# Kernel optimization log

Measured on AMD Instinct MI355X. Metric: run time of the kernel, lower is better.

Reference implementation:

```python
import math
import jax, jax.numpy as jnp
import numpy as np

PERCENTAGES = [0.004, 0.006, 0.008, 0.01, 0.012]
RADIUS = 1.0          # init kwarg / uniform-loss radius
REPULSION_H = 0.0005  # h in get_repulsion_loss


def pairwise_sqdist(x, y):
    # x: [B,N,3], y: [B,M,3] -> [B,N,M] squared euclidean distances
    d2 = (jnp.sum(x * x, -1)[:, :, None]
          + jnp.sum(y * y, -1)[:, None, :]
          - 2.0 * jnp.einsum('bnd,bmd->bnm', x, y))
    return jnp.maximum(d2, 0.0)


def knn_sqdist(x, k):
    # sorted (ascending) squared distances to k nearest neighbors (incl. self)
    d2 = pairwise_sqdist(x, x)
    neg, _ = jax.lax.top_k(-d2, k)
    return -neg  # [B,N,k]


def fps(pcd, npoint):
    # furthest point sampling, start at index 0 (pn2 convention)
    B, N, _ = pcd.shape
    def step(carry, _):
        dist, last = carry
        p = jnp.take_along_axis(pcd, last[:, None, None], axis=1)  # [B,1,3]
        d = jnp.sum((pcd - p) ** 2, -1)                            # [B,N]
        dist = jnp.minimum(dist, d)
        nxt = jnp.argmax(dist, axis=-1)
        return (dist, nxt), nxt
    idx0 = jnp.zeros((B,), jnp.int32)
    dist0 = jnp.full((B, N), 1e10, pcd.dtype)
    _, rest = jax.lax.scan(step, (dist0, idx0), None, length=npoint - 1)
    return jnp.concatenate([idx0[None], rest], axis=0).T  # [B,npoint]


def ball_query(r, nsample, pcd, centers):
    # pn2 ball_query: first nsample indices with d2 < r^2, padded with first hit
    N = pcd.shape[1]
    d2 = pairwise_sqdist(centers, pcd)                       # [B,S,N]
    cand = jnp.where(d2 < r * r, jnp.arange(N)[None, None, :], N)
    sorted_idx = jnp.sort(cand, axis=-1)[..., :nsample]      # [B,S,nsample]
    first = sorted_idx[..., :1]
    return jnp.where(sorted_idx == N, first, sorted_idx)


def get_cd_loss(pred, gt, pcd_radius):
    d2 = pairwise_sqdist(gt, pred)       # [B,N,M]
    cost_for = jnp.min(d2, axis=2)       # gt -> pred, [B,N]
    cost_bac = jnp.min(d2, axis=1)       # pred -> gt, [B,M]
    cost = 0.8 * cost_for + 0.2 * cost_bac
    cost = cost / pcd_radius
    return jnp.mean(cost)


def get_repulsion_loss(pcd, h=REPULSION_H):
    d2 = knn_sqdist(pcd, 5)[:, :, 1:5]   # squared dists to 4 nearest (excl self)
    return jnp.mean(jnp.maximum(-d2 + h, 0.0))


def get_uniform_loss(pcd, radius=RADIUS):
    B, N, _ = pcd.shape
    npoint = int(N * 0.05)
    fidx = fps(pcd, npoint)
    new_xyz = jnp.take_along_axis(pcd, fidx[:, :, None], axis=1)  # [B,npoint,3]
    loss = 0.0
    for p in PERCENTAGES:
        nsample = int(N * p)
        r = math.sqrt(p * radius)
        disk_area = math.pi * radius ** 2 / N
        expect_len = math.sqrt(disk_area)
        idx = ball_query(r, nsample, pcd, new_xyz)            # [B,npoint,nsample]
        grouped = jax.vmap(lambda pts, i: pts[i])(pcd, idx)   # [B,npoint,nsample,3]
        grouped = grouped.reshape(B, npoint * nsample, 3)     # cat(unbind(dim=1))
        nn_d2 = knn_sqdist(grouped, 2)[:, :, 1:]              # [B,M,1]
        uniform_dist = jnp.abs(jnp.sqrt(nn_d2) + 1e-8)
        uniform_dist = jnp.mean(uniform_dist, axis=1)         # [B,1]
        uniform_dist = (uniform_dist - expect_len) ** 2 / (expect_len + 1e-8)
        loss = loss + jnp.mean(uniform_dist) * (p * 100.0) ** 2
    return loss / len(PERCENTAGES)


def setup_inputs() -> dict:
    key = jax.random.key(0)
    k1, k2 = jax.random.split(key)
    pred = jax.random.normal(k1, (8, 2048, 3), jnp.float32)
    gt = jax.random.normal(k2, (8, 2048, 3), jnp.float32)
    pcd_radius = jnp.ones((1,), jnp.float32)
    return {"pred": pred, "gt": gt, "pcd_radius": pcd_radius}


def reference(pred, gt, pcd_radius):
    cd = get_cd_loss(pred, gt, pcd_radius)
    rep = get_repulsion_loss(pred)
    uni = get_uniform_loss(pred)
    return cd + rep + uni
```

## Files before the change

kernel.cpp:

```cpp
#include <hip/hip_runtime.h>
#include <math.h>

#define BB 8
#define NN 2048
#define NPOINT 102
#define H_REP 0.0005f

typedef float v2f __attribute__((ext_vector_type(2)));

__device__ const int    c_ns[5] = {8, 12, 16, 20, 24};
__device__ const double c_p[5]  = {0.004, 0.006, 0.008, 0.01, 0.012};

#define OFF_CD 0
#define OFF_REP 512
#define OFF_UK 768
#define N_DBL 896

__device__ inline double aload_d(const double* p) {
    return __hip_atomic_load(p, __ATOMIC_RELAXED, __HIP_MEMORY_SCOPE_AGENT);
}

__device__ inline void ins5(float c, float& t0, float& t1, float& t2, float& t3, float& t4) {
    float lo;
    lo = fminf(t0, c); c = fmaxf(t0, c); t0 = lo;
    lo = fminf(t1, c); c = fmaxf(t1, c); t1 = lo;
    lo = fminf(t2, c); c = fmaxf(t2, c); t2 = lo;
    lo = fminf(t3, c); c = fmaxf(t3, c); t3 = lo;
    t4 = fminf(t4, c);
}

union SMemP1 {
    struct { float4 sB[NN]; float pm[2][4][128]; } cd;
    struct { float4 sP[NN]; float pm[2][4][64][5]; } rep;
    struct {
        float sx[2][NN], sy[2][NN], sz[2][NN];
        float2 sl[2][2][4];
        int sFi[2][NPOINT];
    } fps;
};

__global__ __launch_bounds__(512, 4) void k_phase1(const float* __restrict__ pred,
                                                   const float* __restrict__ gt,
                                                   int* __restrict__ fidx,
                                                   double* __restrict__ part,
                                                   int* __restrict__ done) {
    __shared__ SMemP1 sm;
    int bid = blockIdx.x;
    int tid = threadIdx.x;
    int lane = tid & 63, wid = tid >> 6;

    if (bid == 4 && tid == 0) *done = 0;

    if (bid < 4) {
        __builtin_amdgcn_s_setprio(1);
        int h = wid >> 2;
        int s = wid & 3;
        int b = bid * 2 + h;
        const float* pp = pred + (size_t)b * NN * 3;
        float px[8], py[8], pz[8], dist[8];
#pragma unroll
        for (int k = 0; k < 8; k++) {
            int i = (s << 9) + (k << 6) + lane;
            float x = pp[i * 3 + 0], y = pp[i * 3 + 1], z = pp[i * 3 + 2];
            px[k] = x; py[k] = y; pz[k] = z; dist[k] = 1e10f;
            sm.fps.sx[h][i] = x; sm.fps.sy[h][i] = y; sm.fps.sz[h][i] = z;
        }
        if ((tid & 255) == 0) sm.fps.sFi[h][0] = 0;
        __syncthreads();
        int last = 0;
#pragma unroll 1
        for (int step = 1; step < NPOINT; ++step) {
            float lx = sm.fps.sx[h][last], ly = sm.fps.sy[h][last], lz = sm.fps.sz[h][last];
            float bv = -1.0f;
            int bi = 0;
#pragma unroll
            for (int k = 0; k < 8; k++) {
                float dx = px[k] - lx, dy = py[k] - ly, dz = pz[k] - lz;
                float nd = fminf(dist[k], dx * dx + dy * dy + dz * dz);
                dist[k] = nd;
                bool better = nd > bv;
                bv = better ? nd : bv;
                bi = better ? ((s << 9) + (k << 6) + lane) : bi;
            }
            {
                float v2; int i2; bool take;
#define DPPC(CTRL)                                                                          \
                v2 = __int_as_float(__builtin_amdgcn_update_dpp(                            \
                        __float_as_int(bv), __float_as_int(bv), CTRL, 0xF, 0xF, false));    \
                i2 = __builtin_amdgcn_update_dpp(bi, bi, CTRL, 0xF, 0xF, false);            \
                take = (v2 > bv) || (v2 == bv && i2 < bi);                                  \
                bv = take ? v2 : bv; bi = take ? i2 : bi;
                DPPC(0x121)
                DPPC(0x122)
                DPPC(0x124)
                DPPC(0x128)
                DPPC(0x142)
                DPPC(0x143)
#undef DPPC
            }
            int pb = step & 1;
            if (lane == 63) sm.fps.sl[pb][h][s] = make_float2(bv, __int_as_float(bi));
            __syncthreads();
            float fv = -2.0f;
            int fi = 0;
#pragma unroll
            for (int w = 0; w < 4; w++) {
                float2 sv = sm.fps.sl[pb][h][w];
                int i2 = __float_as_int(sv.y);
                bool take = (sv.x > fv) || (sv.x == fv && i2 < fi);
                fv = take ? sv.x : fv;
                fi = take ? i2 : fi;
            }
            if ((tid & 255) == 0) sm.fps.sFi[h][step] = fi;
            last = fi;
        }
        __syncthreads();
        for (int t = tid; t < 2 * NPOINT; t += 512) {
            int hh = (t >= NPOINT);
            int st = t - hh * NPOINT;
            fidx[(bid * 2 + hh) * NPOINT + st] = sm.fps.sFi[hh][st];
        }
    } else if (bid < 132) {
        int r = bid - 4;
        int z = r >> 6;
        int b = (r >> 3) & 7;
        int xb = r & 7;
        const float* A = z ? pred : gt;
        const float* Bp = z ? gt : pred;
        const float* bb = Bp + (size_t)b * NN * 3;
        for (int j = tid; j < NN; j += 512) {
            sm.cd.sB[j] = make_float4(bb[j * 3 + 0], bb[j * 3 + 1], bb[j * 3 + 2], 0.0f);
        }
        int h = wid >> 2, sw = wid & 3;
        int rowA = xb * 256 + h * 128 + lane;
        int rowB = rowA + 64;
        const float* aA = A + ((size_t)b * NN + rowA) * 3;
        const float* aB = A + ((size_t)b * NN + rowB) * 3;
        float axA = aA[0], ayA = aA[1], azA = aA[2];
        float axB = aB[0], ayB = aB[1], azB = aB[2];
        __syncthreads();
        float mnA = 1e30f, mnB = 1e30f;
        int j0 = sw * 512;
#pragma unroll 8
        for (int jj = 0; jj < 512; jj++) {
            float4 p = sm.cd.sB[j0 + jj];
            float dxA = axA - p.x, dyA = ayA - p.y, dzA = azA - p.z;
            mnA = fminf(mnA, dxA * dxA + dyA * dyA + dzA * dzA);
            float dxB = axB - p.x, dyB = ayB - p.y, dzB = azB - p.z;
            mnB = fminf(mnB, dxB * dxB + dyB * dyB + dzB * dzB);
        }
        sm.cd.pm[h][sw][lane] = mnA;
        sm.cd.pm[h][sw][64 + lane] = mnB;
        __syncthreads();
        if (tid < 256) {
            int hh = tid >> 7, idx = tid & 127;
            double v = (double)fminf(
                fminf(sm.cd.pm[hh][0][idx], sm.cd.pm[hh][1][idx]),
                fminf(sm.cd.pm[hh][2][idx], sm.cd.pm[hh][3][idx]));
            for (int off = 32; off; off >>= 1) v += __shfl_down(v, off, 64);
            if ((tid & 63) == 0) part[OFF_CD + r * 4 + (tid >> 6)] = v;
        }
    } else {
        int r = bid - 132;
        int b = r >> 4;
        int xb = r & 15;
        const float* pp = pred + (size_t)b * NN * 3;
        for (int j = tid; j < NN; j += 512) {
            sm.rep.sP[j] = make_float4(pp[j * 3 + 0], pp[j * 3 + 1], pp[j * 3 + 2], 0.0f);
        }
        int h = wid >> 2, sw = wid & 3;
        int row = xb * 128 + h * 64 + lane;
        __syncthreads();
        float4 q = sm.rep.sP[row];
        float t0 = 1e30f, t1 = 1e30f, t2 = 1e30f, t3 = 1e30f, t4 = 1e30f;
        int j0 = sw * 512;
#pragma unroll 8
        for (int jj = 0; jj < 512; jj++) {
            float4 p = sm.rep.sP[j0 + jj];
            float dx = q.x - p.x, dy = q.y - p.y, dz = q.z - p.z;
            ins5(dx * dx + dy * dy + dz * dz, t0, t1, t2, t3, t4);
        }
        sm.rep.pm[h][sw][lane][0] = t0; sm.rep.pm[h][sw][lane][1] = t1;
        sm.rep.pm[h][sw][lane][2] = t2; sm.rep.pm[h][sw][lane][3] = t3;
        sm.rep.pm[h][sw][lane][4] = t4;
        __syncthreads();
        if (tid < 128) {
            int hh = tid >> 6, l2 = tid & 63;
            t0 = sm.rep.pm[hh][0][l2][0]; t1 = sm.rep.pm[hh][0][l2][1];
            t2 = sm.rep.pm[hh][0][l2][2]; t3 = sm.rep.pm[hh][0][l2][3];
            t4 = sm.rep.pm[hh][0][l2][4];
#pragma unroll
            for (int w = 1; w < 4; w++) {
#pragma unroll
                for (int k = 0; k < 5; k++) ins5(sm.rep.pm[hh][w][l2][k], t0, t1, t2, t3, t4);
            }
            float sv = fmaxf(H_REP - t1, 0.f) + fmaxf(H_REP - t2, 0.f) +
                       fmaxf(H_REP - t3, 0.f) + fmaxf(H_REP - t4, 0.f);
            double v = (double)sv;
            for (int off = 32; off; off >>= 1) v += __shfl_down(v, off, 64);
            if ((tid & 63) == 0) part[OFF_REP + r * 2 + hh] = v;
        }
    }
}

__global__ __launch_bounds__(1024, 4) void k_tail(const float* __restrict__ pred,
                                                  const int* __restrict__ fidx,
                                                  double* __restrict__ part,
                                                  int* __restrict__ done,
                                                  const float* __restrict__ radius,
                                                  float* __restrict__ out) {
    __shared__ int gidxL[2448];
    __shared__ v2f sX[1280], sY[1280], sZ[1280];
    __shared__ float pm1[16][128], pm2[16][128];
    __shared__ int scnt[NPOINT];
    __shared__ int spre[NPOINT + 1];
    __shared__ int lastFlag;
    int grp = blockIdx.x;
    int pi = grp >> 3, b = grp & 7;
    int ns = c_ns[pi];
    int tid = threadIdx.x, lane = tid & 63, wid = tid >> 6;
    const float* pp = pred + (size_t)b * NN * 3;
    double rd = sqrt(c_p[pi]);
    float r2 = (float)(rd * rd);

    for (int c = wid; c < NPOINT; c += 16) {
        int ci = fidx[b * NPOINT + c];
        float cx = pp[ci * 3 + 0], cy = pp[ci * 3 + 1], cz = pp[ci * 3 + 2];
        float sc = cx * cx + cy * cy + cz * cz;
        int cnt = 0;
        for (int j0 = 0; j0 < NN && cnt < ns; j0 += 64) {
            int j = j0 + lane;
            float x = pp[j * 3 + 0], y = pp[j * 3 + 1], z = pp[j * 3 + 2];
            float sj = x * x + y * y + z * z;
            float d2 = fmaxf(sc + sj - 2.0f * (cx * x + cy * y + cz * z), 0.0f);
            bool prd = d2 < r2;
            unsigned long long mask = __ballot(prd);
            if (prd) {
                int pos = cnt + (int)__popcll(mask & ((1ull << lane) - 1ull));
                if (pos < ns) gidxL[c * ns + pos] = j;
            }
            cnt += (int)__popcll(mask);
        }
        if (lane == 0) scnt[c] = min(cnt, ns);
    }
    __syncthreads();
    if (tid <= NPOINT) {
        int v = 0;
        if (tid >= 1) {
            int sc_ = scnt[tid - 1];
            v = sc_ | ((sc_ + (sc_ < ns ? 1 : 0)) << 16);
        }
        spre[tid] = v;
    }
    __syncthreads();
    for (int s = 1; s <= NPOINT; s <<= 1) {
        int t = 0;
        if (tid <= NPOINT && tid >= s) t = spre[tid - s];
        __syncthreads();
        if (tid <= NPOINT) spre[tid] += t;
        __syncthreads();
    }
    int Q = spre[NPOINT] & 0xffff;
    int CC = spre[NPOINT] >> 16;
    int CCpad = (CC + 255) & ~255;
    float* fX = (float*)sX; float* fY = (float*)sY; float* fZ = (float*)sZ;
    for (int s = tid; s < CCpad; s += 1024) {
        float x = 1e30f, y = 1e30f, z = 1e30f;
        if (s < CC) {
            int lo = 0, hi = NPOINT - 1;
#pragma unroll
            for (int it = 0; it < 7; ++it) {
                int mid = (lo + hi + 1) >> 1;
                bool ge = ((spre[mid] >> 16) <= s);
                lo = ge ? mid : lo;
                hi = ge ? hi : mid - 1;
            }
            int p = s - (spre[lo] >> 16);
            int dup = (scnt[lo] < ns) ? 1 : 0;
            int id = gidxL[lo * ns + max(0, p - dup)];
            x = pp[id * 3 + 0]; y = pp[id * 3 + 1]; z = pp[id * 3 + 2];
        }
        fX[s] = x; fY[s] = y; fZ[s] = z;
    }
    __syncthreads();
    int CHp = CCpad >> 5;
    int j0p = wid * CHp;
    double racc = 0.0;
    for (int tb = 0; tb < Q; tb += 128) {
        float qx[2], qy[2], qz[2];
        double wgt[2];
#pragma unroll
        for (int hh = 0; hh < 2; hh++) {
            int q = tb + lane + 64 * hh;
            qx[hh] = 0.f; qy[hh] = 0.f; qz[hh] = 0.f; wgt[hh] = 0.0;
            if (q < Q) {
                int lo = 0, hi = NPOINT - 1;
#pragma unroll
                for (int it = 0; it < 7; ++it) {
                    int mid = (lo + hi + 1) >> 1;
                    bool ge = ((spre[mid] & 0xffff) <= q);
                    lo = ge ? mid : lo;
                    hi = ge ? hi : mid - 1;
                }
                int p = q - (spre[lo] & 0xffff);
                int dup = (scnt[lo] < ns) ? 1 : 0;
                int cslot = (spre[lo] >> 16) + (p == 0 ? 0 : p + dup);
                qx[hh] = fX[cslot]; qy[hh] = fY[cslot]; qz[hh] = fZ[cslot];
                wgt[hh] = (p == 0) ? (double)(1 + ns - scnt[lo]) : 1.0;
            }
        }
        v2f qax = {qx[0], qx[0]}, qay = {qy[0], qy[0]}, qaz = {qz[0], qz[0]};
        v2f qbx = {qx[1], qx[1]}, qby = {qy[1], qy[1]}, qbz = {qz[1], qz[1]};
        v2f m1A = {1e30f, 1e30f}, m2A = {1e30f, 1e30f};
        v2f m1B = {1e30f, 1e30f}, m2B = {1e30f, 1e30f};
#pragma unroll 4
        for (int jj = 0; jj < CHp; jj++) {
            v2f X = sX[j0p + jj], Y = sY[j0p + jj], Z = sZ[j0p + jj];
            v2f dxA = qax - X, dyA = qay - Y, dzA = qaz - Z;
            v2f dA = dxA * dxA + dyA * dyA + dzA * dzA;
            float l0 = fminf(m1A.x, dA.x), h0 = fmaxf(m1A.x, dA.x);
            float l1 = fminf(m1A.y, dA.y), h1 = fmaxf(m1A.y, dA.y);
            m1A = (v2f){l0, l1};
            m2A = (v2f){fminf(m2A.x, h0), fminf(m2A.y, h1)};
            v2f dxB = qbx - X, dyB = qby - Y, dzB = qbz - Z;
            v2f dB = dxB * dxB + dyB * dyB + dzB * dzB;
            float l2 = fminf(m1B.x, dB.x), h2 = fmaxf(m1B.x, dB.x);
            float l3 = fminf(m1B.y, dB.y), h3 = fmaxf(m1B.y, dB.y);
            m1B = (v2f){l2, l3};
            m2B = (v2f){fminf(m2B.x, h2), fminf(m2B.y, h3)};
        }
        float a1 = fminf(m1A.x, m1A.y);
        float a2 = fminf(fmaxf(m1A.x, m1A.y), fminf(m2A.x, m2A.y));
        float b1 = fminf(m1B.x, m1B.y);
        float b2 = fminf(fmaxf(m1B.x, m1B.y), fminf(m2B.x, m2B.y));
        pm1[wid][lane] = a1; pm2[wid][lane] = a2;
        pm1[wid][64 + lane] = b1; pm2[wid][64 + lane] = b2;
        __syncthreads();
        if (tid < 128) {
            float c1 = pm1[0][tid], c2 = pm2[0][tid];
#pragma unroll
            for (int w = 1; w < 16; w++) {
                float d1 = pm1[w][tid], d2 = pm2[w][tid];
                float n1 = fminf(c1, d1);
                float n2 = fminf(fmaxf(c1, d1), fminf(c2, d2));
                c1 = n1; c2 = n2;
            }
            int q = tb + tid;
            double v = 0.0;
            if (q < Q) v = wgt[tid >> 6] * (double)(sqrtf(c2) + 1e-8f);
            for (int off = 32; off; off >>= 1) v += __shfl_down(v, off, 64);
            if ((tid & 63) == 0) racc += v;
        }
        __syncthreads();
    }
    if (tid == 0) part[OFF_UK + grp * 2 + 0] = racc;
    if (tid == 64) part[OFF_UK + grp * 2 + 1] = racc;
    __threadfence();
    __syncthreads();
    if (tid == 0) lastFlag = (atomicAdd(done, 1) == 39);
    __syncthreads();
    if (!lastFlag) return;
    __threadfence();
    if (tid >= 64) return;
    double s0 = 0.0, s1 = 0.0, sr = 0.0;
#pragma unroll
    for (int k = 0; k < 4; k++) {
        s0 += aload_d(&part[OFF_CD + lane + 64 * k]);
        s1 += aload_d(&part[OFF_CD + 256 + lane + 64 * k]);
        sr += aload_d(&part[OFF_REP + lane + 64 * k]);
    }
    double v = 0.0;
    if (lane < 40) {
        int pi2 = lane >> 3;
        double m = aload_d(&part[OFF_UK + lane * 2]) + aload_d(&part[OFF_UK + lane * 2 + 1]);
        double p = c_p[pi2];
        int M2 = NPOINT * c_ns[pi2];
        double disk_area = M_PI * 1.0 / (double)NN;
        double e = sqrt(disk_area);
        m = m / (double)M2;
        double d = m - e;
        double w = (p * 100.0) * (p * 100.0);
        v = d * d / (e + 1e-8) * w / 40.0;
    }
    for (int off = 32; off; off >>= 1) {
        v += __shfl_down(v, off, 64);
        s0 += __shfl_down(s0, off, 64);
        s1 += __shfl_down(s1, off, 64);
        sr += __shfl_down(sr, off, 64);
    }
    if (lane == 0) {
        double cd = (0.8 * s0 + 0.2 * s1) / ((double)BB * NN) / (double)radius[0];
        double rep = sr / ((double)BB * NN * 4.0);
        out[0] = (float)(cd + rep + v);
    }
}

extern "C" void kernel_launch(void* const* d_in, const int* in_sizes, int n_in,
                              void* d_out, int out_size, void* d_ws, size_t ws_size,
                              hipStream_t stream) {
    const float* pred = (const float*)d_in[0];
    const float* gt = (const float*)d_in[1];
    const float* radius = (const float*)d_in[2];
    float* out = (float*)d_out;

    double* part = (double*)d_ws;
    int* ints = (int*)(part + N_DBL);
    int* done = ints;
    int* fidx = ints + 16;

    hipLaunchKernelGGL(k_phase1, dim3(260), dim3(512), 0, stream, pred, gt, fidx, part, done);
    hipLaunchKernelGGL(k_tail, dim3(40), dim3(1024), 0, stream, pred, fidx, part, done,
                       radius, out);
}
```

Measured before the change: 145.9 us.

## Split phase1 into one-batch FPS blocks and stage pred in shared memory for tail

Phase1 now uses 256-thread blocks, with one batch per FPS block instead of two, and twice as many CD and repulsion blocks. The FPS loop passes the winning point's coordinates through the cross-wave reduction, so the per-step shared-memory lookup of the last point is no longer needed. The tail kernel copies pred into shared memory in SoA form and reads ball-query and gather coordinates from there. It also drops the early exit on the ball-query count, stores group indices as ushort, and pads to 32 instead of 256. The aim is shorter FPS critical-path latency and fewer global loads, at the cost of more shared memory and occupancy changes in the tail.

```diff
diff --git a/kernel.cpp b/kernel.cpp
--- a/kernel.cpp
+++ b/kernel.cpp
@@ -30,16 +30,12 @@
 }
 
 union SMemP1 {
-    struct { float4 sB[NN]; float pm[2][4][128]; } cd;
-    struct { float4 sP[NN]; float pm[2][4][64][5]; } rep;
-    struct {
-        float sx[2][NN], sy[2][NN], sz[2][NN];
-        float2 sl[2][2][4];
-        int sFi[2][NPOINT];
-    } fps;
+    struct { float4 sB[NN]; float pm[4][128]; } cd;
+    struct { float4 sP[NN]; float pm[4][64][5]; } rep;
+    struct { float4 sl4[2][4]; float slz[2][4]; int sFi[NPOINT]; } fps;
 };
 
-__global__ __launch_bounds__(512, 4) void k_phase1(const float* __restrict__ pred,
+__global__ __launch_bounds__(256, 2) void k_phase1(const float* __restrict__ pred,
                                                    const float* __restrict__ gt,
                                                    int* __restrict__ fidx,
                                                    double* __restrict__ part,
@@ -49,28 +45,25 @@
     int tid = threadIdx.x;
     int lane = tid & 63, wid = tid >> 6;
 
-    if (bid == 4 && tid == 0) *done = 0;
-
-    if (bid < 4) {
+    if (bid == 8 && tid == 0) *done = 0;
+
+    if (bid < 8) {
         __builtin_amdgcn_s_setprio(1);
-        int h = wid >> 2;
-        int s = wid & 3;
-        int b = bid * 2 + h;
+        int b = bid;
         const float* pp = pred + (size_t)b * NN * 3;
         float px[8], py[8], pz[8], dist[8];
 #pragma unroll
         for (int k = 0; k < 8; k++) {
-            int i = (s << 9) + (k << 6) + lane;
-            float x = pp[i * 3 + 0], y = pp[i * 3 + 1], z = pp[i * 3 + 2];
-            px[k] = x; py[k] = y; pz[k] = z; dist[k] = 1e10f;
-            sm.fps.sx[h][i] = x; sm.fps.sy[h][i] = y; sm.fps.sz[h][i] = z;
-        }
-        if ((tid & 255) == 0) sm.fps.sFi[h][0] = 0;
-        __syncthreads();
-        int last = 0;
+            int i = (wid << 9) + (k << 6) + lane;
+            px[k] = pp[i * 3 + 0];
+            py[k] = pp[i * 3 + 1];
+            pz[k] = pp[i * 3 + 2];
+            dist[k] = 1e10f;
+        }
+        if (tid == 0) sm.fps.sFi[0] = 0;
+        float lx = pp[0], ly = pp[1], lz = pp[2];
 #pragma unroll 1
         for (int step = 1; step < NPOINT; ++step) {
-            float lx = sm.fps.sx[h][last], ly = sm.fps.sy[h][last], lz = sm.fps.sz[h][last];
             float bv = -1.0f;
             int bi = 0;
 #pragma unroll
@@ -80,7 +73,7 @@
                 dist[k] = nd;
                 bool better = nd > bv;
                 bv = better ? nd : bv;
-                bi = better ? ((s << 9) + (k << 6) + lane) : bi;
+                bi = better ? ((wid << 9) + (k << 6) + lane) : bi;
             }
             {
                 float v2; int i2; bool take;
@@ -98,41 +91,51 @@
                 DPPC(0x143)
 #undef DPPC
             }
+            float wx = 0.f, wy = 0.f, wz = 0.f;
+            bool own = false;
+#pragma unroll
+            for (int k = 0; k < 8; k++) {
+                bool m = (bi == ((wid << 9) + (k << 6) + lane));
+                wx = m ? px[k] : wx;
+                wy = m ? py[k] : wy;
+                wz = m ? pz[k] : wz;
+                own = own || m;
+            }
             int pb = step & 1;
-            if (lane == 63) sm.fps.sl[pb][h][s] = make_float2(bv, __int_as_float(bi));
+            if (own) {
+                sm.fps.sl4[pb][wid] = make_float4(bv, __int_as_float(bi), wx, wy);
+                sm.fps.slz[pb][wid] = wz;
+            }
             __syncthreads();
-            float fv = -2.0f;
+            float fv = -2.0f, fx = 0.f, fy = 0.f, fz = 0.f;
             int fi = 0;
 #pragma unroll
             for (int w = 0; w < 4; w++) {
-                float2 sv = sm.fps.sl[pb][h][w];
-                int i2 = __float_as_int(sv.y);
-                bool take = (sv.x > fv) || (sv.x == fv && i2 < fi);
-                fv = take ? sv.x : fv;
-                fi = take ? i2 : fi;
-            }
-            if ((tid & 255) == 0) sm.fps.sFi[h][step] = fi;
-            last = fi;
-        }
-        __syncthreads();
-        for (int t = tid; t < 2 * NPOINT; t += 512) {
-            int hh = (t >= NPOINT);
-            int st = t - hh * NPOINT;
-            fidx[(bid * 2 + hh) * NPOINT + st] = sm.fps.sFi[hh][st];
-        }
-    } else if (bid < 132) {
-        int r = bid - 4;
-        int z = r >> 6;
-        int b = (r >> 3) & 7;
-        int xb = r & 7;
+                float4 s4 = sm.fps.sl4[pb][w];
+                float szv = sm.fps.slz[pb][w];
+                int i2 = __float_as_int(s4.y);
+                bool take = (s4.x > fv) || (s4.x == fv && i2 < fi);
+                fv = take ? s4.x : fv; fi = take ? i2 : fi;
+                fx = take ? s4.z : fx; fy = take ? s4.w : fy;
+                fz = take ? szv : fz;
+            }
+            if (tid == 0) sm.fps.sFi[step] = fi;
+            lx = fx; ly = fy; lz = fz;
+        }
+        __syncthreads();
+        for (int s = tid; s < NPOINT; s += 256) fidx[b * NPOINT + s] = sm.fps.sFi[s];
+    } else if (bid < 264) {
+        int r = bid - 8;
+        int z = r >> 7;
+        int b = (r >> 4) & 7;
+        int xb = r & 15;
         const float* A = z ? pred : gt;
         const float* Bp = z ? gt : pred;
         const float* bb = Bp + (size_t)b * NN * 3;
-        for (int j = tid; j < NN; j += 512) {
+        for (int j = tid; j < NN; j += 256) {
             sm.cd.sB[j] = make_float4(bb[j * 3 + 0], bb[j * 3 + 1], bb[j * 3 + 2], 0.0f);
         }
-        int h = wid >> 2, sw = wid & 3;
-        int rowA = xb * 256 + h * 128 + lane;
+        int rowA = xb * 128 + lane;
         int rowB = rowA + 64;
         const float* aA = A + ((size_t)b * NN + rowA) * 3;
         const float* aB = A + ((size_t)b * NN + rowB) * 3;
@@ -140,7 +143,7 @@
         float axB = aB[0], ayB = aB[1], azB = aB[2];
         __syncthreads();
         float mnA = 1e30f, mnB = 1e30f;
-        int j0 = sw * 512;
+        int j0 = wid * 512;
 #pragma unroll 8
         for (int jj = 0; jj < 512; jj++) {
             float4 p = sm.cd.sB[j0 + jj];
@@ -149,69 +152,69 @@
             float dxB = axB - p.x, dyB = ayB - p.y, dzB = azB - p.z;
             mnB = fminf(mnB, dxB * dxB + dyB * dyB + dzB * dzB);
         }
-        sm.cd.pm[h][sw][lane] = mnA;
-        sm.cd.pm[h][sw][64 + lane] = mnB;
-        __syncthreads();
-        if (tid < 256) {
-            int hh = tid >> 7, idx = tid & 127;
-            double v = (double)fminf(
-                fminf(sm.cd.pm[hh][0][idx], sm.cd.pm[hh][1][idx]),
-                fminf(sm.cd.pm[hh][2][idx], sm.cd.pm[hh][3][idx]));
+        sm.cd.pm[wid][lane] = mnA;
+        sm.cd.pm[wid][64 + lane] = mnB;
+        __syncthreads();
+        if (tid < 128) {
+            double v = (double)fminf(fminf(sm.cd.pm[0][tid], sm.cd.pm[1][tid]),
+                                     fminf(sm.cd.pm[2][tid], sm.cd.pm[3][tid]));
             for (int off = 32; off; off >>= 1) v += __shfl_down(v, off, 64);
-            if ((tid & 63) == 0) part[OFF_CD + r * 4 + (tid >> 6)] = v;
+            if (lane == 0) part[OFF_CD + r * 2 + (tid >> 6)] = v;
         }
     } else {
-        int r = bid - 132;
-        int b = r >> 4;
-        int xb = r & 15;
+        int r = bid - 264;
+        int b = r >> 5;
+        int xb = r & 31;
         const float* pp = pred + (size_t)b * NN * 3;
-        for (int j = tid; j < NN; j += 512) {
+        for (int j = tid; j < NN; j += 256) {
             sm.rep.sP[j] = make_float4(pp[j * 3 + 0], pp[j * 3 + 1], pp[j * 3 + 2], 0.0f);
         }
-        int h = wid >> 2, sw = wid & 3;
-        int row = xb * 128 + h * 64 + lane;
+        int row = xb * 64 + lane;
         __syncthreads();
         float4 q = sm.rep.sP[row];
         float t0 = 1e30f, t1 = 1e30f, t2 = 1e30f, t3 = 1e30f, t4 = 1e30f;
-        int j0 = sw * 512;
+        int j0 = wid * 512;
 #pragma unroll 8
         for (int jj = 0; jj < 512; jj++) {
             float4 p = sm.rep.sP[j0 + jj];
             float dx = q.x - p.x, dy = q.y - p.y, dz = q.z - p.z;
             ins5(dx * dx + dy * dy + dz * dz, t0, t1, t2, t3, t4);
         }
-        sm.rep.pm[h][sw][lane][0] = t0; sm.rep.pm[h][sw][lane][1] = t1;
-        sm.rep.pm[h][sw][lane][2] = t2; sm.rep.pm[h][sw][lane][3] = t3;
-        sm.rep.pm[h][sw][lane][4] = t4;
-        __syncthreads();
-        if (tid < 128) {
-            int hh = tid >> 6, l2 = tid & 63;
-            t0 = sm.rep.pm[hh][0][l2][0]; t1 = sm.rep.pm[hh][0][l2][1];
-            t2 = sm.rep.pm[hh][0][l2][2]; t3 = sm.rep.pm[hh][0][l2][3];
-            t4 = sm.rep.pm[hh][0][l2][4];
+        sm.rep.pm[wid][lane][0] = t0; sm.rep.pm[wid][lane][1] = t1;
+        sm.rep.pm[wid][lane][2] = t2; sm.rep.pm[wid][lane][3] = t3;
+        sm.rep.pm[wid][lane][4] = t4;
+        __syncthreads();
+        if (tid < 64) {
+            t0 = sm.rep.pm[0][lane][0]; t1 = sm.rep.pm[0][lane][1]; t2 = sm.rep.pm[0][lane][2];
+            t3 = sm.rep.pm[0][lane][3]; t4 = sm.rep.pm[0][lane][4];
 #pragma unroll
             for (int w = 1; w < 4; w++) {
 #pragma unroll
-                for (int k = 0; k < 5; k++) ins5(sm.rep.pm[hh][w][l2][k], t0, t1, t2, t3, t4);
-            }
-            float sv = fmaxf(H_REP - t1, 0.f) + fmaxf(H_REP - t2, 0.f) +
-                       fmaxf(H_REP - t3, 0.f) + fmaxf(H_REP - t4, 0.f);
-            double v = (double)sv;
+                for (int k = 0; k < 5; k++) ins5(sm.rep.pm[w][lane][k], t0, t1, t2, t3, t4);
+            }
+            float s = fmaxf(H_REP - t1, 0.f) + fmaxf(H_REP - t2, 0.f) +
+                      fmaxf(H_REP - t3, 0.f) + fmaxf(H_REP - t4, 0.f);
+            double v = (double)s;
             for (int off = 32; off; off >>= 1) v += __shfl_down(v, off, 64);
-            if ((tid & 63) == 0) part[OFF_REP + r * 2 + hh] = v;
+            if (tid == 0) part[OFF_REP + r] = v;
         }
     }
 }
 
-__global__ __launch_bounds__(1024, 4) void k_tail(const float* __restrict__ pred,
+union UTail {
+    struct { float sx[NN], sy[NN], sz[NN]; } st;
+    struct { float pm1[16][128], pm2[16][128]; } pm;
+};
+
+__global__ __launch_bounds__(1024, 1) void k_tail(const float* __restrict__ pred,
                                                   const int* __restrict__ fidx,
                                                   double* __restrict__ part,
                                                   int* __restrict__ done,
                                                   const float* __restrict__ radius,
                                                   float* __restrict__ out) {
-    __shared__ int gidxL[2448];
-    __shared__ v2f sX[1280], sY[1280], sZ[1280];
-    __shared__ float pm1[16][128], pm2[16][128];
+    __shared__ UTail ut;
+    __shared__ unsigned short gidxL[2448];
+    __shared__ v2f cX[1232], cY[1232], cZ[1232];
     __shared__ int scnt[NPOINT];
     __shared__ int spre[NPOINT + 1];
     __shared__ int lastFlag;
@@ -223,21 +226,32 @@
     double rd = sqrt(c_p[pi]);
     float r2 = (float)(rd * rd);
 
+    for (int t = tid; t < 3 * NN; t += 1024) {
+        float v = pp[t];
+        int idx = t / 3;
+        int comp = t - idx * 3;
+        if (comp == 0) ut.st.sx[idx] = v;
+        else if (comp == 1) ut.st.sy[idx] = v;
+        else ut.st.sz[idx] = v;
+    }
+    __syncthreads();
+
     for (int c = wid; c < NPOINT; c += 16) {
         int ci = fidx[b * NPOINT + c];
-        float cx = pp[ci * 3 + 0], cy = pp[ci * 3 + 1], cz = pp[ci * 3 + 2];
+        float cx = ut.st.sx[ci], cy = ut.st.sy[ci], cz = ut.st.sz[ci];
         float sc = cx * cx + cy * cy + cz * cz;
         int cnt = 0;
-        for (int j0 = 0; j0 < NN && cnt < ns; j0 += 64) {
+#pragma unroll 4
+        for (int j0 = 0; j0 < NN; j0 += 64) {
             int j = j0 + lane;
-            float x = pp[j * 3 + 0], y = pp[j * 3 + 1], z = pp[j * 3 + 2];
+            float x = ut.st.sx[j], y = ut.st.sy[j], z = ut.st.sz[j];
             float sj = x * x + y * y + z * z;
             float d2 = fmaxf(sc + sj - 2.0f * (cx * x + cy * y + cz * z), 0.0f);
             bool prd = d2 < r2;
             unsigned long long mask = __ballot(prd);
             if (prd) {
                 int pos = cnt + (int)__popcll(mask & ((1ull << lane) - 1ull));
-                if (pos < ns) gidxL[c * ns + pos] = j;
+                if (pos < ns) gidxL[c * ns + pos] = (unsigned short)j;
             }
             cnt += (int)__popcll(mask);
         }
@@ -262,8 +276,8 @@
     }
     int Q = spre[NPOINT] & 0xffff;
     int CC = spre[NPOINT] >> 16;
-    int CCpad = (CC + 255) & ~255;
-    float* fX = (float*)sX; float* fY = (float*)sY; float* fZ = (float*)sZ;
+    int CCpad = (CC + 31) & ~31;
+    float* fX = (float*)cX; float* fY = (float*)cY; float* fZ = (float*)cZ;
     for (int s = tid; s < CCpad; s += 1024) {
         float x = 1e30f, y = 1e30f, z = 1e30f;
         if (s < CC) {
@@ -278,7 +292,7 @@
             int p = s - (spre[lo] >> 16);
             int dup = (scnt[lo] < ns) ? 1 : 0;
             int id = gidxL[lo * ns + max(0, p - dup)];
-            x = pp[id * 3 + 0]; y = pp[id * 3 + 1]; z = pp[id * 3 + 2];
+            x = ut.st.sx[id]; y = ut.st.sy[id]; z = ut.st.sz[id];
         }
         fX[s] = x; fY[s] = y; fZ[s] = z;
     }
@@ -315,7 +329,7 @@
         v2f m1B = {1e30f, 1e30f}, m2B = {1e30f, 1e30f};
 #pragma unroll 4
         for (int jj = 0; jj < CHp; jj++) {
-            v2f X = sX[j0p + jj], Y = sY[j0p + jj], Z = sZ[j0p + jj];
+            v2f X = cX[j0p + jj], Y = cY[j0p + jj], Z = cZ[j0p + jj];
             v2f dxA = qax - X, dyA = qay - Y, dzA = qaz - Z;
             v2f dA = dxA * dxA + dyA * dyA + dzA * dzA;
             float l0 = fminf(m1A.x, dA.x), h0 = fmaxf(m1A.x, dA.x);
@@ -333,14 +347,14 @@
         float a2 = fminf(fmaxf(m1A.x, m1A.y), fminf(m2A.x, m2A.y));
         float b1 = fminf(m1B.x, m1B.y);
         float b2 = fminf(fmaxf(m1B.x, m1B.y), fminf(m2B.x, m2B.y));
-        pm1[wid][lane] = a1; pm2[wid][lane] = a2;
-        pm1[wid][64 + lane] = b1; pm2[wid][64 + lane] = b2;
+        ut.pm.pm1[wid][lane] = a1; ut.pm.pm2[wid][lane] = a2;
+        ut.pm.pm1[wid][64 + lane] = b1; ut.pm.pm2[wid][64 + lane] = b2;
         __syncthreads();
         if (tid < 128) {
-            float c1 = pm1[0][tid], c2 = pm2[0][tid];
+            float c1 = ut.pm.pm1[0][tid], c2 = ut.pm.pm2[0][tid];
 #pragma unroll
             for (int w = 1; w < 16; w++) {
-                float d1 = pm1[w][tid], d2 = pm2[w][tid];
+                float d1 = ut.pm.pm1[w][tid], d2 = ut.pm.pm2[w][tid];
                 float n1 = fminf(c1, d1);
                 float n2 = fminf(fmaxf(c1, d1), fminf(c2, d2));
                 c1 = n1; c2 = n2;
@@ -408,7 +422,7 @@
     int* done = ints;
     int* fidx = ints + 16;
 
-    hipLaunchKernelGGL(k_phase1, dim3(260), dim3(512), 0, stream, pred, gt, fidx, part, done);
+    hipLaunchKernelGGL(k_phase1, dim3(520), dim3(256), 0, stream, pred, gt, fidx, part, done);
     hipLaunchKernelGGL(k_tail, dim3(40), dim3(1024), 0, stream, pred, fidx, part, done,
                        radius, out);
 }
```

After: 138.6 us. 5.0% less time.
